# Optimization experiments

Hardware: AMD Instinct MI355X
Metric: run time of the kernel (lower is better)

Reference implementation:

```python
import jax, jax.numpy as jnp
import numpy as np

DIM = 256
WS = 7
NUM_HEADS = 8
NW = 4096


def _relative_position_index(ws: int) -> jnp.ndarray:
    coords = jnp.stack(jnp.meshgrid(jnp.arange(ws), jnp.arange(ws), indexing='ij'))  # [2, ws, ws]
    flat = coords.reshape(2, -1)                                # [2, N]
    rel = flat[:, :, None] - flat[:, None, :]                   # [2, N, N]
    rel = rel.transpose(1, 2, 0) + (ws - 1)                     # [N, N, 2]
    rel = rel.at[:, :, 0].multiply(2 * ws - 1)
    return rel.sum(-1).astype(jnp.int32)                        # [N, N]


def setup_inputs() -> dict:
    key = jax.random.key(0)
    ks = jax.random.split(key, 7)
    N = WS * WS
    x_win = jax.random.normal(ks[0], (NW, N, DIM), dtype=jnp.float32)
    attn_mask = jnp.zeros((NW, N, N), dtype=jnp.float32)
    w_qkv = jax.random.normal(ks[1], (3 * DIM, DIM), dtype=jnp.float32) * (1.0 / np.sqrt(DIM))
    b_qkv = jax.random.normal(ks[2], (3 * DIM,), dtype=jnp.float32) * 0.02
    w_proj = jax.random.normal(ks[3], (DIM, DIM), dtype=jnp.float32) * (1.0 / np.sqrt(DIM))
    b_proj = jax.random.normal(ks[4], (DIM,), dtype=jnp.float32) * 0.02
    bias_table = jax.random.normal(ks[5], ((2 * WS - 1) * (2 * WS - 1), NUM_HEADS), dtype=jnp.float32)
    rel_index = _relative_position_index(WS)
    return {
        'x_win': x_win, 'attn_mask': attn_mask,
        'w_qkv': w_qkv, 'b_qkv': b_qkv,
        'w_proj': w_proj, 'b_proj': b_proj,
        'bias_table': bias_table, 'rel_index': rel_index,
    }


def reference(x_win, attn_mask, w_qkv, b_qkv, w_proj, b_proj, bias_table, rel_index):
    nW, N, C = x_win.shape
    H = bias_table.shape[-1]
    head_dim = C // H
    scale = 1.0 / np.sqrt(head_dim).astype(np.float32)

    # QKV projection (eqx.nn.Linear: y = W x + b)
    qkv = jnp.einsum('wnc,oc->wno', x_win, w_qkv) + b_qkv      # [nW, N, 3C]
    q, k, v = jnp.split(qkv, 3, axis=-1)

    def to_heads(t):
        return t.reshape(nW, N, H, head_dim).transpose(0, 2, 1, 3)  # [nW, H, N, d]

    q, k, v = to_heads(q), to_heads(k), to_heads(v)

    attn = jnp.einsum('whnd,whmd->whnm', q * scale, k)          # [nW, H, N, N]

    # Gathered relative position bias -> [H, N, N]
    bias = bias_table[rel_index.reshape(-1)].reshape(N, N, H).transpose(2, 0, 1)
    attn = attn + bias[None, :, :, :] + attn_mask[:, None, :, :]
    attn = jax.nn.softmax(attn, axis=-1)

    out = jnp.einsum('whnm,whmd->whnd', attn, v)                # [nW, H, N, d]
    out = out.transpose(0, 2, 1, 3).reshape(nW, N, C)
    out = jnp.einsum('wnc,oc->wno', out, w_proj) + b_proj
    return out
```

## Files before the change

kernel.cpp:

```cpp
#include <hip/hip_runtime.h>
#include <hip/hip_bf16.h>

typedef __bf16 bf16;
typedef bf16 bf16x4 __attribute__((ext_vector_type(4)));
typedef bf16 bf16x8 __attribute__((ext_vector_type(8)));
typedef float f32x4 __attribute__((ext_vector_type(4)));

#define MFMA16(a, b, c) __builtin_amdgcn_mfma_f32_16x16x32_bf16((a), (b), (c), 0, 0, 0)

constexpr float kScale = 0.17677669529663687f;

constexpr int WQKV_OFF = 0;
constexpr int WPROJ_OFF = 393216;
constexpr int BIAS_OFF = 524288;
constexpr int BQKV_OFF = 601120;

constexpr int QK_OFF = 26240;
constexpr int QS = 410;
constexpr int LDS_BYTES = 78720;

__global__ void prep_kernel(const float* __restrict__ w_qkv, const float* __restrict__ b_qkv,
                            const float* __restrict__ w_proj, const float* __restrict__ bias_table,
                            const int* __restrict__ rel_index, char* __restrict__ ws) {
  int i = blockIdx.x * 256 + threadIdx.x;
  bf16* wqkvb = (bf16*)(ws + WQKV_OFF);
  bf16* wprojb = (bf16*)(ws + WPROJ_OFF);
  float* biasx = (float*)(ws + BIAS_OFF);
  float* bqs = (float*)(ws + BQKV_OFF);
  if (i < 196608) {
    float v = w_qkv[i];
    if (i < 65536) v *= kScale;
    wqkvb[i] = (bf16)v;
  } else if (i < 262144) {
    int j = i - 196608;
    wprojb[j] = (bf16)w_proj[j];
  } else if (i < 281352) {
    int j = i - 262144;
    int h = j / 2401, nm = j - h * 2401;
    int mm = nm / 49, nn = nm - mm * 49;
    biasx[j] = bias_table[rel_index[nn * 49 + mm] * 8 + h];
  } else if (i < 282120) {
    int j = i - 281352;
    bqs[j] = b_qkv[j] * (j < 256 ? kScale : 1.0f);
  }
}

__device__ __forceinline__ bf16x8 xpose8(f32x4 lo, f32x4 hi, int base, bool glow) {
  bf16x8 f;
#pragma unroll
  for (int i = 0; i < 4; ++i) {
    float a0 = __shfl(lo[i], base);
    float a1 = __shfl(lo[i], base + 16);
    float b0 = __shfl(hi[i], base);
    float b1 = __shfl(hi[i], base + 16);
    f[i] = (bf16)(glow ? a0 : b0);
    f[i + 4] = (bf16)(glow ? a1 : b1);
  }
  return f;
}

__global__ __launch_bounds__(256, 2) void attn_kernel(
    const float* __restrict__ x, const float* __restrict__ mask, const float* __restrict__ b_proj,
    const char* __restrict__ ws, float* __restrict__ out) {
  extern __shared__ char smem[];
  bf16* xb = (bf16*)(smem);
  bf16* qk = (bf16*)(smem + QK_OFF);
  float* outf = (float*)(smem + QK_OFF);

  const bf16* wqkvb = (const bf16*)(ws + WQKV_OFF);
  const bf16* wprojb = (const bf16*)(ws + WPROJ_OFF);
  const float* biasx = (const float*)(ws + BIAS_OFF);
  const float* bqs = (const float*)(ws + BQKV_OFF);

  const int tid = threadIdx.x;
  const int w = blockIdx.x;
  const int lane = tid & 63;
  const int wave = tid >> 6;
  const int g = lane >> 4;
  const int c = lane & 15;

  const float* xw = x + (size_t)w * 12544;

#pragma unroll
  for (int it = 0; it < 13; ++it) {
    int idx = it * 256 + tid;
    if (idx < 3136) {
      int n = idx >> 6, c4 = (idx & 63) << 2;
      float4 v = ((const float4*)xw)[idx];
      bf16x4 b4;
      b4[0] = (bf16)v.x; b4[1] = (bf16)v.y; b4[2] = (bf16)v.z; b4[3] = (bf16)v.w;
      *(bf16x4*)(xb + ((c4 >> 3) * QS + n * 8 + (c4 & 7))) = b4;
    }
  }
  __syncthreads();

  for (int qd = 0; qd < 2; ++qd) {
    const int ot0 = wave * 8 + qd * 4;
    f32x4 acc[4][4] = {};
#pragma unroll
    for (int ks = 0; ks < 8; ++ks) {
      bf16x8 b[4];
#pragma unroll
      for (int nt = 0; nt < 4; ++nt)
        b[nt] = *(const bf16x8*)(xb + (ks * 4 + g) * QS + c * 8 + nt * 128);
      bf16x8 a[4];
#pragma unroll
      for (int t = 0; t < 4; ++t)
        a[t] = *(const bf16x8*)(wqkvb + ((ot0 + t) * 16 + c) * 256 + ks * 32 + g * 8);
#pragma unroll
      for (int t = 0; t < 4; ++t)
#pragma unroll
        for (int nt = 0; nt < 4; ++nt) acc[t][nt] = MFMA16(a[t], b[nt], acc[t][nt]);
    }
#pragma unroll
    for (int t = 0; t < 4; ++t) {
      const int ot = ot0 + t;
      const int ob = ot * 16 + g * 4;
      const float bq0 = bqs[ob], bq1 = bqs[ob + 1], bq2 = bqs[ob + 2], bq3 = bqs[ob + 3];
      const int oc = ob >> 3, olow = ob & 7;
#pragma unroll
      for (int nt = 0; nt < 4; ++nt) {
        int n = nt * 16 + c;
        if (n < 50) {
          bool ok = (n < 49);
          bf16x4 pk;
          pk[0] = ok ? (bf16)(acc[t][nt][0] + bq0) : (bf16)0.f;
          pk[1] = ok ? (bf16)(acc[t][nt][1] + bq1) : (bf16)0.f;
          pk[2] = ok ? (bf16)(acc[t][nt][2] + bq2) : (bf16)0.f;
          pk[3] = ok ? (bf16)(acc[t][nt][3] + bq3) : (bf16)0.f;
          *(bf16x4*)(qk + (oc * QS + n * 8 + olow)) = pk;
        }
      }
    }
  }

  const int base = (g & 1) * 32 + c;
  const bool glow = (g < 2);

  bf16x8 va[2][2][2];
  {
    f32x4 acc[4][4] = {};
#pragma unroll
    for (int ks = 0; ks < 8; ++ks) {
      bf16x8 a[4];
#pragma unroll
      for (int mt = 0; mt < 4; ++mt)
        a[mt] = *(const bf16x8*)(xb + (ks * 4 + g) * QS + c * 8 + mt * 128);
      bf16x8 bw[4];
#pragma unroll
      for (int t = 0; t < 4; ++t)
        bw[t] = *(const bf16x8*)(wqkvb + (512 + (wave * 4 + t) * 16 + c) * 256 + ks * 32 + g * 8);
#pragma unroll
      for (int t = 0; t < 4; ++t)
#pragma unroll
        for (int mt = 0; mt < 4; ++mt) acc[t][mt] = MFMA16(a[mt], bw[t], acc[t][mt]);
    }
#pragma unroll
    for (int t = 0; t < 4; ++t) {
      const int o = 512 + (wave * 4 + t) * 16 + c;
      const float bv = bqs[o];
#pragma unroll
      for (int mt = 0; mt < 4; ++mt) {
        acc[t][mt][0] += bv; acc[t][mt][1] += bv; acc[t][mt][2] += bv; acc[t][mt][3] += bv;
      }
#pragma unroll
      for (int ks = 0; ks < 2; ++ks) {
        bf16x8 f = xpose8(acc[t][2 * ks], acc[t][2 * ks + 1], base, glow);
#pragma unroll
        for (int j = 0; j < 8; ++j) {
          int m = ks * 32 + g * 8 + j;
          if (m >= 49) f[j] = (bf16)0.f;
        }
        va[t >> 1][t & 1][ks] = f;
      }
    }
  }
  __syncthreads();

  const float* mk = mask + (size_t)w * 2401;

#pragma unroll
  for (int hh = 0; hh < 2; ++hh) {
    const int h = wave * 2 + hh;
    const float* bhT = biasx + h * 2401;

    bf16x8 qa[4], kb[4];
#pragma unroll
    for (int rt = 0; rt < 4; ++rt) {
      int n = rt * 16 + c; n = n > 49 ? 49 : n;
      qa[rt] = *(const bf16x8*)(qk + ((h * 4 + g) * QS + n * 8));
    }
#pragma unroll
    for (int mt = 0; mt < 4; ++mt) {
      int m = mt * 16 + c; m = m > 49 ? 49 : m;
      kb[mt] = *(const bf16x8*)(qk + ((32 + h * 4 + g) * QS + m * 8));
    }

    f32x4 s[4][4] = {};
#pragma unroll
    for (int mt = 0; mt < 4; ++mt)
#pragma unroll
      for (int nt = 0; nt < 4; ++nt) s[mt][nt] = MFMA16(kb[mt], qa[nt], s[mt][nt]);

    float bi[16], mi[16];
#define GATHER(NT)                                              \
    {                                                           \
      const int n_ = (NT) * 16 + c;                             \
      const int nc_ = n_ > 48 ? 48 : n_;                        \
      _Pragma("unroll") for (int mt = 0; mt < 4; ++mt)          \
        _Pragma("unroll") for (int i = 0; i < 4; ++i) {         \
          int m_ = mt * 16 + g * 4 + i;                         \
          int mc_ = m_ > 48 ? 48 : m_;                          \
          bi[mt * 4 + i] = bhT[mc_ * 49 + nc_];                 \
          mi[mt * 4 + i] = mk[nc_ * 49 + mc_];                  \
        }                                                       \
    }

    GATHER(0);
    f32x4 oacc[2][4] = {};
#pragma unroll
    for (int nt = 0; nt < 4; ++nt) {
      const int n = nt * 16 + c;
      const bool nok = (n < 49);
      float p[4][4];
      float sum = 0.f;
#pragma unroll
      for (int mt = 0; mt < 4; ++mt)
#pragma unroll
        for (int i = 0; i < 4; ++i) {
          int m = mt * 16 + g * 4 + i;
          float v = s[mt][nt][i] + bi[mt * 4 + i] + mi[mt * 4 + i];
          float pv = (nok && m < 49) ? __expf(v) : 0.f;
          p[mt][i] = pv;
          sum += pv;
        }
      sum += __shfl_xor(sum, 16);
      sum += __shfl_xor(sum, 32);
      float rinv = nok ? (1.0f / sum) : 0.0f;
#pragma unroll
      for (int mt = 0; mt < 4; ++mt)
#pragma unroll
        for (int i = 0; i < 4; ++i) p[mt][i] *= rinv;

      if (nt < 3) {
        if (nt == 0) GATHER(1);
        if (nt == 1) GATHER(2);
        if (nt == 2) GATHER(3);
      }

#pragma unroll
      for (int ks = 0; ks < 2; ++ks) {
        bf16x8 f;
#pragma unroll
        for (int j = 0; j < 8; ++j) {
          int src = ((g & 1) * 2 + (j >> 2)) * 16 + c;
          float vA = __shfl(p[2 * ks][j & 3], src);
          float vB = __shfl(p[2 * ks + 1][j & 3], src);
          f[j] = (bf16)(glow ? vA : vB);
        }
#pragma unroll
        for (int dt = 0; dt < 2; ++dt) oacc[dt][nt] = MFMA16(va[hh][dt][ks], f, oacc[dt][nt]);
      }
    }
#undef GATHER

#pragma unroll
    for (int dt = 0; dt < 2; ++dt) {
      int cb = h * 32 + dt * 16 + g * 4;
      int cc = cb >> 3, clow = cb & 7;
#pragma unroll
      for (int nt = 0; nt < 4; ++nt) {
        int n = nt * 16 + c;
        if (n < 49) {
          bf16x4 pk;
          pk[0] = (bf16)oacc[dt][nt][0]; pk[1] = (bf16)oacc[dt][nt][1];
          pk[2] = (bf16)oacc[dt][nt][2]; pk[3] = (bf16)oacc[dt][nt][3];
          *(bf16x4*)(xb + (cc * QS + n * 8 + clow)) = pk;
        }
      }
    }
  }
  __syncthreads();

  {
    f32x4 acc[4][4] = {};
#pragma unroll
    for (int ks = 0; ks < 8; ++ks) {
      bf16x8 a[4];
#pragma unroll
      for (int mt = 0; mt < 4; ++mt)
        a[mt] = *(const bf16x8*)(xb + (ks * 4 + g) * QS + c * 8 + mt * 128);
      bf16x8 bw[4];
#pragma unroll
      for (int t = 0; t < 4; ++t)
        bw[t] = *(const bf16x8*)(wprojb + ((wave * 4 + t) * 16 + c) * 256 + ks * 32 + g * 8);
#pragma unroll
      for (int t = 0; t < 4; ++t)
#pragma unroll
        for (int mt = 0; mt < 4; ++mt) acc[t][mt] = MFMA16(a[mt], bw[t], acc[t][mt]);
    }
#pragma unroll
    for (int t = 0; t < 4; ++t) {
      const int ct = wave * 4 + t;
      const float bp = b_proj[ct * 16 + c];
      const int co = ct * 16 + c, q = co >> 2, c3 = co & 3;
#pragma unroll
      for (int mt = 0; mt < 4; ++mt) {
#pragma unroll
        for (int i = 0; i < 4; ++i) {
          int n = mt * 16 + g * 4 + i;
          if (n < 49) outf[n * 256 + ((q ^ (n & 15)) << 2) + c3] = acc[t][mt][i] + bp;
        }
      }
    }
  }
  __syncthreads();

  float4* outw4 = (float4*)(out + (size_t)w * 12544);
  const float4* outf4 = (const float4*)outf;
#pragma unroll
  for (int it = 0; it < 13; ++it) {
    int f = it * 256 + tid;
    if (f < 3136) {
      int n = f >> 6, q = f & 63;
      outw4[f] = outf4[n * 64 + (q ^ (n & 15))];
    }
  }
}

extern "C" void kernel_launch(void* const* d_in, const int* in_sizes, int n_in,
                              void* d_out, int out_size, void* d_ws, size_t ws_size,
                              hipStream_t stream) {
  const float* x = (const float*)d_in[0];
  const float* mask = (const float*)d_in[1];
  const float* w_qkv = (const float*)d_in[2];
  const float* b_qkv = (const float*)d_in[3];
  const float* w_proj = (const float*)d_in[4];
  const float* b_proj = (const float*)d_in[5];
  const float* bias_table = (const float*)d_in[6];
  const int* rel_index = (const int*)d_in[7];
  float* out = (float*)d_out;
  char* ws = (char*)d_ws;

  (void)in_sizes; (void)n_in; (void)out_size; (void)ws_size;

  hipFuncSetAttribute((const void*)attn_kernel, hipFuncAttributeMaxDynamicSharedMemorySize,
                      LDS_BYTES);

  prep_kernel<<<1103, 256, 0, stream>>>(w_qkv, b_qkv, w_proj, bias_table, rel_index, ws);
  attn_kernel<<<4096, 256, LDS_BYTES, stream>>>(x, mask, b_proj, ws, out);
}
```

Measured before the change: 443.9 us.

## Compute Q/K per head in registers to shrink LDS and raise occupancy

Drops the LDS buffer that held the Q and K projections for all heads. Each wave now computes its head's Q and K tiles inside the head loop and transposes them in registers with shuffles. The output projection is split into two halves so its staging buffer fits in the x region. LDS drops from about 77KB to about 52KB and launch bounds go from 2 to 3 blocks per CU, aiming at higher occupancy and latency hiding. The trade-off is extra shuffle work, one more barrier per half, and tighter register limits that could cause spills.

```diff
diff --git a/kernel.cpp b/kernel.cpp
--- a/kernel.cpp
+++ b/kernel.cpp
@@ -15,9 +15,10 @@
 constexpr int BIAS_OFF = 524288;
 constexpr int BQKV_OFF = 601120;
 
-constexpr int QK_OFF = 26240;
+constexpr int A_OFF = 0;
+constexpr int B_OFF = 26240;
 constexpr int QS = 410;
-constexpr int LDS_BYTES = 78720;
+constexpr int LDS_BYTES = 52736;
 
 __global__ void prep_kernel(const float* __restrict__ w_qkv, const float* __restrict__ b_qkv,
                             const float* __restrict__ w_proj, const float* __restrict__ bias_table,
@@ -59,13 +60,13 @@
   return f;
 }
 
-__global__ __launch_bounds__(256, 2) void attn_kernel(
+__global__ __launch_bounds__(256, 3) void attn_kernel(
     const float* __restrict__ x, const float* __restrict__ mask, const float* __restrict__ b_proj,
     const char* __restrict__ ws, float* __restrict__ out) {
   extern __shared__ char smem[];
-  bf16* xb = (bf16*)(smem);
-  bf16* qk = (bf16*)(smem + QK_OFF);
-  float* outf = (float*)(smem + QK_OFF);
+  bf16* xb = (bf16*)(smem + A_OFF);
+  bf16* ao = (bf16*)(smem + B_OFF);
+  float* outf = (float*)(smem + A_OFF);
 
   const bf16* wqkvb = (const bf16*)(ws + WQKV_OFF);
   const bf16* wprojb = (const bf16*)(ws + WPROJ_OFF);
@@ -94,46 +95,6 @@
   }
   __syncthreads();
 
-  for (int qd = 0; qd < 2; ++qd) {
-    const int ot0 = wave * 8 + qd * 4;
-    f32x4 acc[4][4] = {};
-#pragma unroll
-    for (int ks = 0; ks < 8; ++ks) {
-      bf16x8 b[4];
-#pragma unroll
-      for (int nt = 0; nt < 4; ++nt)
-        b[nt] = *(const bf16x8*)(xb + (ks * 4 + g) * QS + c * 8 + nt * 128);
-      bf16x8 a[4];
-#pragma unroll
-      for (int t = 0; t < 4; ++t)
-        a[t] = *(const bf16x8*)(wqkvb + ((ot0 + t) * 16 + c) * 256 + ks * 32 + g * 8);
-#pragma unroll
-      for (int t = 0; t < 4; ++t)
-#pragma unroll
-        for (int nt = 0; nt < 4; ++nt) acc[t][nt] = MFMA16(a[t], b[nt], acc[t][nt]);
-    }
-#pragma unroll
-    for (int t = 0; t < 4; ++t) {
-      const int ot = ot0 + t;
-      const int ob = ot * 16 + g * 4;
-      const float bq0 = bqs[ob], bq1 = bqs[ob + 1], bq2 = bqs[ob + 2], bq3 = bqs[ob + 3];
-      const int oc = ob >> 3, olow = ob & 7;
-#pragma unroll
-      for (int nt = 0; nt < 4; ++nt) {
-        int n = nt * 16 + c;
-        if (n < 50) {
-          bool ok = (n < 49);
-          bf16x4 pk;
-          pk[0] = ok ? (bf16)(acc[t][nt][0] + bq0) : (bf16)0.f;
-          pk[1] = ok ? (bf16)(acc[t][nt][1] + bq1) : (bf16)0.f;
-          pk[2] = ok ? (bf16)(acc[t][nt][2] + bq2) : (bf16)0.f;
-          pk[3] = ok ? (bf16)(acc[t][nt][3] + bq3) : (bf16)0.f;
-          *(bf16x4*)(qk + (oc * QS + n * 8 + olow)) = pk;
-        }
-      }
-    }
-  }
-
   const int base = (g & 1) * 32 + c;
   const bool glow = (g < 2);
 
@@ -175,25 +136,49 @@
       }
     }
   }
-  __syncthreads();
 
   const float* mk = mask + (size_t)w * 2401;
 
-#pragma unroll
+#pragma unroll 1
   for (int hh = 0; hh < 2; ++hh) {
     const int h = wave * 2 + hh;
     const float* bhT = biasx + h * 2401;
 
     bf16x8 qa[4], kb[4];
-#pragma unroll
-    for (int rt = 0; rt < 4; ++rt) {
-      int n = rt * 16 + c; n = n > 49 ? 49 : n;
-      qa[rt] = *(const bf16x8*)(qk + ((h * 4 + g) * QS + n * 8));
-    }
-#pragma unroll
-    for (int mt = 0; mt < 4; ++mt) {
-      int m = mt * 16 + c; m = m > 49 ? 49 : m;
-      kb[mt] = *(const bf16x8*)(qk + ((32 + h * 4 + g) * QS + m * 8));
+    {
+      const int ob0 = 256 + h * 32;
+      const int ob2 = h * 32;
+      f32x4 acc[4][4] = {};
+#pragma unroll
+      for (int ks = 0; ks < 8; ++ks) {
+        bf16x8 b[4];
+#pragma unroll
+        for (int nt = 0; nt < 4; ++nt)
+          b[nt] = *(const bf16x8*)(xb + (ks * 4 + g) * QS + c * 8 + nt * 128);
+        bf16x8 a[4];
+        a[0] = *(const bf16x8*)(wqkvb + ((ob0 + c) * 256) + ks * 32 + g * 8);
+        a[1] = *(const bf16x8*)(wqkvb + ((ob0 + 16 + c) * 256) + ks * 32 + g * 8);
+        a[2] = *(const bf16x8*)(wqkvb + ((ob2 + c) * 256) + ks * 32 + g * 8);
+        a[3] = *(const bf16x8*)(wqkvb + ((ob2 + 16 + c) * 256) + ks * 32 + g * 8);
+#pragma unroll
+        for (int t = 0; t < 4; ++t)
+#pragma unroll
+          for (int nt = 0; nt < 4; ++nt) acc[t][nt] = MFMA16(a[t], b[nt], acc[t][nt]);
+      }
+#pragma unroll
+      for (int t = 0; t < 4; ++t) {
+        const int ob = (t < 2 ? ob0 + t * 16 : ob2 + (t - 2) * 16) + g * 4;
+#pragma unroll
+        for (int i = 0; i < 4; ++i) {
+          float bq = bqs[ob + i];
+#pragma unroll
+          for (int nt = 0; nt < 4; ++nt) acc[t][nt][i] += bq;
+        }
+      }
+#pragma unroll
+      for (int mt = 0; mt < 4; ++mt) kb[mt] = xpose8(acc[0][mt], acc[1][mt], base, glow);
+#pragma unroll
+      for (int rt = 0; rt < 4; ++rt) qa[rt] = xpose8(acc[2][rt], acc[3][rt], base, glow);
     }
 
     f32x4 s[4][4] = {};
@@ -275,56 +260,60 @@
           bf16x4 pk;
           pk[0] = (bf16)oacc[dt][nt][0]; pk[1] = (bf16)oacc[dt][nt][1];
           pk[2] = (bf16)oacc[dt][nt][2]; pk[3] = (bf16)oacc[dt][nt][3];
-          *(bf16x4*)(xb + (cc * QS + n * 8 + clow)) = pk;
+          *(bf16x4*)(ao + (cc * QS + n * 8 + clow)) = pk;
         }
       }
     }
   }
   __syncthreads();
 
-  {
-    f32x4 acc[4][4] = {};
+  float4* outw4 = (float4*)(out + (size_t)w * 12544);
+  const float4* outf4 = (const float4*)outf;
+#pragma unroll 1
+  for (int half = 0; half < 2; ++half) {
+    f32x4 acc[2][4] = {};
 #pragma unroll
     for (int ks = 0; ks < 8; ++ks) {
       bf16x8 a[4];
 #pragma unroll
       for (int mt = 0; mt < 4; ++mt)
-        a[mt] = *(const bf16x8*)(xb + (ks * 4 + g) * QS + c * 8 + mt * 128);
-      bf16x8 bw[4];
-#pragma unroll
-      for (int t = 0; t < 4; ++t)
-        bw[t] = *(const bf16x8*)(wprojb + ((wave * 4 + t) * 16 + c) * 256 + ks * 32 + g * 8);
-#pragma unroll
-      for (int t = 0; t < 4; ++t)
-#pragma unroll
-        for (int mt = 0; mt < 4; ++mt) acc[t][mt] = MFMA16(a[mt], bw[t], acc[t][mt]);
-    }
-#pragma unroll
-    for (int t = 0; t < 4; ++t) {
-      const int ct = wave * 4 + t;
+        a[mt] = *(const bf16x8*)(ao + (ks * 4 + g) * QS + c * 8 + mt * 128);
+      bf16x8 bw[2];
+#pragma unroll
+      for (int tt = 0; tt < 2; ++tt)
+        bw[tt] = *(const bf16x8*)(wprojb +
+                                  ((half * 8 + wave * 2 + tt) * 16 + c) * 256 + ks * 32 + g * 8);
+#pragma unroll
+      for (int tt = 0; tt < 2; ++tt)
+#pragma unroll
+        for (int mt = 0; mt < 4; ++mt) acc[tt][mt] = MFMA16(a[mt], bw[tt], acc[tt][mt]);
+    }
+#pragma unroll
+    for (int tt = 0; tt < 2; ++tt) {
+      const int ctl = wave * 2 + tt;
+      const int ct = half * 8 + ctl;
       const float bp = b_proj[ct * 16 + c];
-      const int co = ct * 16 + c, q = co >> 2, c3 = co & 3;
+      const int q = ctl * 4 + (c >> 2);
+      const int c3 = c & 3;
 #pragma unroll
       for (int mt = 0; mt < 4; ++mt) {
 #pragma unroll
         for (int i = 0; i < 4; ++i) {
           int n = mt * 16 + g * 4 + i;
-          if (n < 49) outf[n * 256 + ((q ^ (n & 15)) << 2) + c3] = acc[t][mt][i] + bp;
-        }
-      }
-    }
-  }
-  __syncthreads();
-
-  float4* outw4 = (float4*)(out + (size_t)w * 12544);
-  const float4* outf4 = (const float4*)outf;
-#pragma unroll
-  for (int it = 0; it < 13; ++it) {
-    int f = it * 256 + tid;
-    if (f < 3136) {
-      int n = f >> 6, q = f & 63;
-      outw4[f] = outf4[n * 64 + (q ^ (n & 15))];
-    }
+          if (n < 49) outf[n * 128 + ((q ^ (n & 7)) << 2) + c3] = acc[tt][mt][i] + bp;
+        }
+      }
+    }
+    __syncthreads();
+#pragma unroll
+    for (int it = 0; it < 7; ++it) {
+      int f = it * 256 + tid;
+      if (f < 1568) {
+        int n = f >> 5, q2 = f & 31;
+        outw4[n * 64 + half * 32 + q2] = outf4[n * 32 + (q2 ^ (n & 7))];
+      }
+    }
+    __syncthreads();
   }
 }
 
```

New measurement: 656.5 us. 47.9% more time.

## Split fused window attention into Q/K projection and attention kernels with global staging

Applied to the files above, without the earlier changes.

Q and K projections move to a separate kernel that writes bf16 Q/K tiles into workspace in chunks of windows. A second kernel recomputes V, then does attention and the output projection with a smaller LDS footprint, so it can run more blocks per CU. The aim is higher occupancy and less LDS pressure than the single fused kernel. The cost is extra global traffic for Q/K, a second read of x, and more launches. If the workspace is too small it falls back to the original fused kernel.

```diff
diff --git a/kernel.cpp b/kernel.cpp
--- a/kernel.cpp
+++ b/kernel.cpp
@@ -14,10 +14,10 @@
 constexpr int WPROJ_OFF = 393216;
 constexpr int BIAS_OFF = 524288;
 constexpr int BQKV_OFF = 601120;
-
-constexpr int QK_OFF = 26240;
+constexpr size_t QKG_OFF = 604672;
+
 constexpr int QS = 410;
-constexpr int LDS_BYTES = 78720;
+constexpr int GQS = 400;
 
 __global__ void prep_kernel(const float* __restrict__ w_qkv, const float* __restrict__ b_qkv,
                             const float* __restrict__ w_proj, const float* __restrict__ bias_table,
@@ -59,28 +59,7 @@
   return f;
 }
 
-__global__ __launch_bounds__(256, 2) void attn_kernel(
-    const float* __restrict__ x, const float* __restrict__ mask, const float* __restrict__ b_proj,
-    const char* __restrict__ ws, float* __restrict__ out) {
-  extern __shared__ char smem[];
-  bf16* xb = (bf16*)(smem);
-  bf16* qk = (bf16*)(smem + QK_OFF);
-  float* outf = (float*)(smem + QK_OFF);
-
-  const bf16* wqkvb = (const bf16*)(ws + WQKV_OFF);
-  const bf16* wprojb = (const bf16*)(ws + WPROJ_OFF);
-  const float* biasx = (const float*)(ws + BIAS_OFF);
-  const float* bqs = (const float*)(ws + BQKV_OFF);
-
-  const int tid = threadIdx.x;
-  const int w = blockIdx.x;
-  const int lane = tid & 63;
-  const int wave = tid >> 6;
-  const int g = lane >> 4;
-  const int c = lane & 15;
-
-  const float* xw = x + (size_t)w * 12544;
-
+__device__ __forceinline__ void stage_x(const float* __restrict__ xw, bf16* xb, int tid) {
 #pragma unroll
   for (int it = 0; it < 13; ++it) {
     int idx = it * 256 + tid;
@@ -92,6 +71,309 @@
       *(bf16x4*)(xb + ((c4 >> 3) * QS + n * 8 + (c4 & 7))) = b4;
     }
   }
+}
+
+__global__ __launch_bounds__(256, 4) void qk_kernel(
+    const float* __restrict__ x, const char* __restrict__ ws, bf16* __restrict__ qkg, int w0) {
+  __shared__ bf16 xb[32 * QS + 128];
+  const bf16* wqkvb = (const bf16*)(ws + WQKV_OFF);
+  const float* bqs = (const float*)(ws + BQKV_OFF);
+
+  const int tid = threadIdx.x;
+  const int lane = tid & 63;
+  const int wave = tid >> 6;
+  const int g = lane >> 4;
+  const int c = lane & 15;
+
+  stage_x(x + (size_t)(w0 + blockIdx.x) * 12544, xb, tid);
+  __syncthreads();
+
+  bf16* qw = qkg + (size_t)blockIdx.x * 25600;
+
+  for (int qd = 0; qd < 2; ++qd) {
+    const int ot0 = wave * 8 + qd * 4;
+    f32x4 acc[4][4] = {};
+#pragma unroll
+    for (int ks = 0; ks < 8; ++ks) {
+      bf16x8 b[4];
+#pragma unroll
+      for (int nt = 0; nt < 4; ++nt)
+        b[nt] = *(const bf16x8*)(xb + (ks * 4 + g) * QS + c * 8 + nt * 128);
+      bf16x8 a[4];
+#pragma unroll
+      for (int t = 0; t < 4; ++t)
+        a[t] = *(const bf16x8*)(wqkvb + ((ot0 + t) * 16 + c) * 256 + ks * 32 + g * 8);
+#pragma unroll
+      for (int t = 0; t < 4; ++t)
+#pragma unroll
+        for (int nt = 0; nt < 4; ++nt) acc[t][nt] = MFMA16(a[t], b[nt], acc[t][nt]);
+    }
+#pragma unroll
+    for (int t = 0; t < 4; ++t) {
+      const int ot = ot0 + t;
+      const int ob = ot * 16 + g * 4;
+      const float bq0 = bqs[ob], bq1 = bqs[ob + 1], bq2 = bqs[ob + 2], bq3 = bqs[ob + 3];
+      const int oc = ob >> 3, olow = ob & 7;
+#pragma unroll
+      for (int nt = 0; nt < 4; ++nt) {
+        int n = nt * 16 + c;
+        if (n < 50) {
+          bool ok = (n < 49);
+          bf16x4 pk;
+          pk[0] = ok ? (bf16)(acc[t][nt][0] + bq0) : (bf16)0.f;
+          pk[1] = ok ? (bf16)(acc[t][nt][1] + bq1) : (bf16)0.f;
+          pk[2] = ok ? (bf16)(acc[t][nt][2] + bq2) : (bf16)0.f;
+          pk[3] = ok ? (bf16)(acc[t][nt][3] + bq3) : (bf16)0.f;
+          *(bf16x4*)(qw + (oc * GQS + n * 8 + olow)) = pk;
+        }
+      }
+    }
+  }
+}
+
+__global__ __launch_bounds__(256, 3) void attn2_kernel(
+    const float* __restrict__ x, const float* __restrict__ mask, const float* __restrict__ b_proj,
+    const char* __restrict__ ws, const bf16* __restrict__ qkg, float* __restrict__ out, int w0) {
+  __shared__ char smem[26240 + 25088 + 128];
+  bf16* xb = (bf16*)smem;
+  float* outf = (float*)(smem + 26240);
+
+  const bf16* wqkvb = (const bf16*)(ws + WQKV_OFF);
+  const bf16* wprojb = (const bf16*)(ws + WPROJ_OFF);
+  const float* biasx = (const float*)(ws + BIAS_OFF);
+  const float* bqs = (const float*)(ws + BQKV_OFF);
+
+  const int tid = threadIdx.x;
+  const int w = w0 + blockIdx.x;
+  const int lane = tid & 63;
+  const int wave = tid >> 6;
+  const int g = lane >> 4;
+  const int c = lane & 15;
+
+  stage_x(x + (size_t)w * 12544, xb, tid);
+  __syncthreads();
+
+  const int base = (g & 1) * 32 + c;
+  const bool glow = (g < 2);
+
+  bf16x8 va[2][2][2];
+  {
+    f32x4 acc[4][4] = {};
+#pragma unroll
+    for (int ks = 0; ks < 8; ++ks) {
+      bf16x8 a[4];
+#pragma unroll
+      for (int mt = 0; mt < 4; ++mt)
+        a[mt] = *(const bf16x8*)(xb + (ks * 4 + g) * QS + c * 8 + mt * 128);
+      bf16x8 bw[4];
+#pragma unroll
+      for (int t = 0; t < 4; ++t)
+        bw[t] = *(const bf16x8*)(wqkvb + (512 + (wave * 4 + t) * 16 + c) * 256 + ks * 32 + g * 8);
+#pragma unroll
+      for (int t = 0; t < 4; ++t)
+#pragma unroll
+        for (int mt = 0; mt < 4; ++mt) acc[t][mt] = MFMA16(a[mt], bw[t], acc[t][mt]);
+    }
+#pragma unroll
+    for (int t = 0; t < 4; ++t) {
+      const int o = 512 + (wave * 4 + t) * 16 + c;
+      const float bv = bqs[o];
+#pragma unroll
+      for (int mt = 0; mt < 4; ++mt) {
+        acc[t][mt][0] += bv; acc[t][mt][1] += bv; acc[t][mt][2] += bv; acc[t][mt][3] += bv;
+      }
+#pragma unroll
+      for (int ks = 0; ks < 2; ++ks) {
+        bf16x8 f = xpose8(acc[t][2 * ks], acc[t][2 * ks + 1], base, glow);
+#pragma unroll
+        for (int j = 0; j < 8; ++j) {
+          int m = ks * 32 + g * 8 + j;
+          if (m >= 49) f[j] = (bf16)0.f;
+        }
+        va[t >> 1][t & 1][ks] = f;
+      }
+    }
+  }
+  __syncthreads();
+  bf16* ao = xb;
+
+  const float* mk = mask + (size_t)w * 2401;
+  const bf16* qw = qkg + (size_t)blockIdx.x * 25600;
+
+#pragma unroll
+  for (int hh = 0; hh < 2; ++hh) {
+    const int h = wave * 2 + hh;
+    const float* bhT = biasx + h * 2401;
+
+    bf16x8 qa[4], kb[4];
+#pragma unroll
+    for (int rt = 0; rt < 4; ++rt) {
+      int n = rt * 16 + c; n = n > 49 ? 49 : n;
+      qa[rt] = *(const bf16x8*)(qw + (h * 4 + g) * GQS + n * 8);
+    }
+#pragma unroll
+    for (int mt = 0; mt < 4; ++mt) {
+      int m = mt * 16 + c; m = m > 49 ? 49 : m;
+      kb[mt] = *(const bf16x8*)(qw + ((32 + h * 4 + g) * GQS + m * 8));
+    }
+
+    f32x4 s[4][4] = {};
+#pragma unroll
+    for (int mt = 0; mt < 4; ++mt)
+#pragma unroll
+      for (int nt = 0; nt < 4; ++nt) s[mt][nt] = MFMA16(kb[mt], qa[nt], s[mt][nt]);
+
+    float bi[16], mi[16];
+#define GATHER(NT)                                              \
+    {                                                           \
+      const int n_ = (NT) * 16 + c;                             \
+      const int nc_ = n_ > 48 ? 48 : n_;                        \
+      _Pragma("unroll") for (int mt = 0; mt < 4; ++mt)          \
+        _Pragma("unroll") for (int i = 0; i < 4; ++i) {         \
+          int m_ = mt * 16 + g * 4 + i;                         \
+          int mc_ = m_ > 48 ? 48 : m_;                          \
+          bi[mt * 4 + i] = bhT[mc_ * 49 + nc_];                 \
+          mi[mt * 4 + i] = mk[nc_ * 49 + mc_];                  \
+        }                                                       \
+    }
+
+    GATHER(0);
+    f32x4 oacc[2][4] = {};
+#pragma unroll
+    for (int nt = 0; nt < 4; ++nt) {
+      const int n = nt * 16 + c;
+      const bool nok = (n < 49);
+      float p[4][4];
+      float sum = 0.f;
+#pragma unroll
+      for (int mt = 0; mt < 4; ++mt)
+#pragma unroll
+        for (int i = 0; i < 4; ++i) {
+          int m = mt * 16 + g * 4 + i;
+          float v = s[mt][nt][i] + bi[mt * 4 + i] + mi[mt * 4 + i];
+          float pv = (nok && m < 49) ? __expf(v) : 0.f;
+          p[mt][i] = pv;
+          sum += pv;
+        }
+      sum += __shfl_xor(sum, 16);
+      sum += __shfl_xor(sum, 32);
+      float rinv = nok ? (1.0f / sum) : 0.0f;
+#pragma unroll
+      for (int mt = 0; mt < 4; ++mt)
+#pragma unroll
+        for (int i = 0; i < 4; ++i) p[mt][i] *= rinv;
+
+      if (nt < 3) {
+        if (nt == 0) GATHER(1);
+        if (nt == 1) GATHER(2);
+        if (nt == 2) GATHER(3);
+      }
+
+#pragma unroll
+      for (int ks = 0; ks < 2; ++ks) {
+        bf16x8 f;
+#pragma unroll
+        for (int j = 0; j < 8; ++j) {
+          int src = ((g & 1) * 2 + (j >> 2)) * 16 + c;
+          float vA = __shfl(p[2 * ks][j & 3], src);
+          float vB = __shfl(p[2 * ks + 1][j & 3], src);
+          f[j] = (bf16)(glow ? vA : vB);
+        }
+#pragma unroll
+        for (int dt = 0; dt < 2; ++dt) oacc[dt][nt] = MFMA16(va[hh][dt][ks], f, oacc[dt][nt]);
+      }
+    }
+#undef GATHER
+
+#pragma unroll
+    for (int dt = 0; dt < 2; ++dt) {
+      int cb = h * 32 + dt * 16 + g * 4;
+      int cc = cb >> 3, clow = cb & 7;
+#pragma unroll
+      for (int nt = 0; nt < 4; ++nt) {
+        int n = nt * 16 + c;
+        if (n < 49) {
+          bf16x4 pk;
+          pk[0] = (bf16)oacc[dt][nt][0]; pk[1] = (bf16)oacc[dt][nt][1];
+          pk[2] = (bf16)oacc[dt][nt][2]; pk[3] = (bf16)oacc[dt][nt][3];
+          *(bf16x4*)(ao + (cc * QS + n * 8 + clow)) = pk;
+        }
+      }
+    }
+  }
+  __syncthreads();
+
+  float4* outw4 = (float4*)(out + (size_t)w * 12544);
+  const float4* outf4 = (const float4*)outf;
+#pragma unroll 1
+  for (int half = 0; half < 2; ++half) {
+    f32x4 acc[2][4] = {};
+#pragma unroll
+    for (int ks = 0; ks < 8; ++ks) {
+      bf16x8 a[4];
+#pragma unroll
+      for (int mt = 0; mt < 4; ++mt)
+        a[mt] = *(const bf16x8*)(ao + (ks * 4 + g) * QS + c * 8 + mt * 128);
+      bf16x8 bw[2];
+#pragma unroll
+      for (int tt = 0; tt < 2; ++tt)
+        bw[tt] = *(const bf16x8*)(wprojb +
+                                  ((half * 8 + wave * 2 + tt) * 16 + c) * 256 + ks * 32 + g * 8);
+#pragma unroll
+      for (int tt = 0; tt < 2; ++tt)
+#pragma unroll
+        for (int mt = 0; mt < 4; ++mt) acc[tt][mt] = MFMA16(a[mt], bw[tt], acc[tt][mt]);
+    }
+#pragma unroll
+    for (int tt = 0; tt < 2; ++tt) {
+      const int ctl = wave * 2 + tt;
+      const int ct = half * 8 + ctl;
+      const float bp = b_proj[ct * 16 + c];
+      const int q = ctl * 4 + (c >> 2);
+      const int c3 = c & 3;
+#pragma unroll
+      for (int mt = 0; mt < 4; ++mt) {
+#pragma unroll
+        for (int i = 0; i < 4; ++i) {
+          int n = mt * 16 + g * 4 + i;
+          if (n < 49) outf[n * 128 + ((q ^ (n & 7)) << 2) + c3] = acc[tt][mt][i] + bp;
+        }
+      }
+    }
+    __syncthreads();
+#pragma unroll
+    for (int it = 0; it < 7; ++it) {
+      int f = it * 256 + tid;
+      if (f < 1568) {
+        int n = f >> 5, q2 = f & 31;
+        outw4[n * 64 + half * 32 + q2] = outf4[n * 32 + (q2 ^ (n & 7))];
+      }
+    }
+    __syncthreads();
+  }
+}
+
+__global__ __launch_bounds__(256, 2) void fused_kernel(
+    const float* __restrict__ x, const float* __restrict__ mask, const float* __restrict__ b_proj,
+    const char* __restrict__ ws, float* __restrict__ out) {
+  extern __shared__ char dsm[];
+  bf16* xb = (bf16*)(dsm);
+  bf16* qk = (bf16*)(dsm + 26240);
+  float* outf = (float*)(dsm + 26240);
+
+  const bf16* wqkvb = (const bf16*)(ws + WQKV_OFF);
+  const bf16* wprojb = (const bf16*)(ws + WPROJ_OFF);
+  const float* biasx = (const float*)(ws + BIAS_OFF);
+  const float* bqs = (const float*)(ws + BQKV_OFF);
+
+  const int tid = threadIdx.x;
+  const int w = blockIdx.x;
+  const int lane = tid & 63;
+  const int wave = tid >> 6;
+  const int g = lane >> 4;
+  const int c = lane & 15;
+
+  stage_x(x + (size_t)w * 12544, xb, tid);
   __syncthreads();
 
   for (int qd = 0; qd < 2; ++qd) {
@@ -342,11 +624,24 @@
   float* out = (float*)d_out;
   char* ws = (char*)d_ws;
 
-  (void)in_sizes; (void)n_in; (void)out_size; (void)ws_size;
-
-  hipFuncSetAttribute((const void*)attn_kernel, hipFuncAttributeMaxDynamicSharedMemorySize,
-                      LDS_BYTES);
+  (void)in_sizes; (void)n_in; (void)out_size;
 
   prep_kernel<<<1103, 256, 0, stream>>>(w_qkv, b_qkv, w_proj, bias_table, rel_index, ws);
-  attn_kernel<<<4096, 256, LDS_BYTES, stream>>>(x, mask, b_proj, ws, out);
+
+  size_t avail = ws_size > QKG_OFF ? ws_size - QKG_OFF : 0;
+  long cwl = (long)(avail / 51200);
+  int cw = cwl > 1024 ? 1024 : (int)cwl;
+
+  if (cw >= 512) {
+    bf16* qkg = (bf16*)(ws + QKG_OFF);
+    for (int s = 0; s < 4096; s += cw) {
+      int nb = (4096 - s) < cw ? (4096 - s) : cw;
+      qk_kernel<<<nb, 256, 0, stream>>>(x, ws, qkg, s);
+      attn2_kernel<<<nb, 256, 0, stream>>>(x, mask, b_proj, ws, qkg, out, s);
+    }
+  } else {
+    hipFuncSetAttribute((const void*)fused_kernel, hipFuncAttributeMaxDynamicSharedMemorySize,
+                        78720);
+    fused_kernel<<<4096, 256, 78720, stream>>>(x, mask, b_proj, ws, out);
+  }
 }
```

New measurement: 685.8 us. 54.5% more time.

## Pre-permute bias and mask into MFMA fragment order for coalesced loads

Applied to the files above, without the earlier changes.

The relative-position bias table is now expanded in the prep kernel into a per-head, per-lane layout that matches the MFMA accumulator fragments. A new kernel converts each window's mask to bf16 in the same fragment order. The attention kernel can then read bias and mask with contiguous lane-indexed loads instead of transposed, strided gathers. The cost is an extra full pass over the mask, with a read and a bf16 write to the workspace, plus reduced mask precision.

```diff
diff --git a/kernel.cpp b/kernel.cpp
--- a/kernel.cpp
+++ b/kernel.cpp
@@ -12,10 +12,10 @@
 
 constexpr int WQKV_OFF = 0;
 constexpr int WPROJ_OFF = 393216;
-constexpr int BIAS_OFF = 524288;
-constexpr int BQKV_OFF = 601120;
-
-constexpr int QK_OFF = 26240;
+constexpr int BIASR_OFF = 524288;
+constexpr int BQKV_OFF = 655360;
+constexpr size_t MASKR_OFF = 658432;
+
 constexpr int QS = 410;
 constexpr int LDS_BYTES = 78720;
 
@@ -25,7 +25,7 @@
   int i = blockIdx.x * 256 + threadIdx.x;
   bf16* wqkvb = (bf16*)(ws + WQKV_OFF);
   bf16* wprojb = (bf16*)(ws + WPROJ_OFF);
-  float* biasx = (float*)(ws + BIAS_OFF);
+  float* biasr = (float*)(ws + BIASR_OFF);
   float* bqs = (float*)(ws + BQKV_OFF);
   if (i < 196608) {
     float v = w_qkv[i];
@@ -34,14 +34,38 @@
   } else if (i < 262144) {
     int j = i - 196608;
     wprojb[j] = (bf16)w_proj[j];
-  } else if (i < 281352) {
+  } else if (i < 294912) {
     int j = i - 262144;
-    int h = j / 2401, nm = j - h * 2401;
-    int mm = nm / 49, nn = nm - mm * 49;
-    biasx[j] = bias_table[rel_index[nn * 49 + mm] * 8 + h];
-  } else if (i < 282120) {
-    int j = i - 281352;
+    int h = j >> 12, r = j & 4095;
+    int lane = r & 63, q = r >> 6;
+    int i2 = q & 3, p = q >> 2, mt = p & 3, nt = p >> 2;
+    int nn = nt * 16 + (lane & 15); nn = nn > 48 ? 48 : nn;
+    int mm = mt * 16 + (lane >> 4) * 4 + i2; mm = mm > 48 ? 48 : mm;
+    biasr[j] = bias_table[rel_index[nn * 49 + mm] * 8 + h];
+  } else if (i < 295680) {
+    int j = i - 294912;
     bqs[j] = b_qkv[j] * (j < 256 ? kScale : 1.0f);
+  }
+}
+
+__global__ void maskr_kernel(const float* __restrict__ mask, char* __restrict__ ws) {
+  const int w = blockIdx.x;
+  const float* mk = mask + (size_t)w * 2401;
+  bf16* mr = (bf16*)(ws + MASKR_OFF) + (size_t)w * 4096;
+#pragma unroll
+  for (int rep = 0; rep < 4; ++rep) {
+    int o = (rep * 256 + threadIdx.x) * 4;
+    int q = o >> 6;
+    int i2 = q & 3, p = q >> 2, mt = p & 3, nt = p >> 2;
+    bf16x4 v;
+#pragma unroll
+    for (int j = 0; j < 4; ++j) {
+      int L = (o & 63) + j;
+      int nn = nt * 16 + (L & 15); nn = nn > 48 ? 48 : nn;
+      int mm = mt * 16 + (L >> 4) * 4 + i2; mm = mm > 48 ? 48 : mm;
+      v[j] = (bf16)mk[nn * 49 + mm];
+    }
+    *(bf16x4*)(mr + o) = v;
   }
 }
 
@@ -60,16 +84,16 @@
 }
 
 __global__ __launch_bounds__(256, 2) void attn_kernel(
-    const float* __restrict__ x, const float* __restrict__ mask, const float* __restrict__ b_proj,
+    const float* __restrict__ x, const float* __restrict__ b_proj,
     const char* __restrict__ ws, float* __restrict__ out) {
   extern __shared__ char smem[];
   bf16* xb = (bf16*)(smem);
-  bf16* qk = (bf16*)(smem + QK_OFF);
-  float* outf = (float*)(smem + QK_OFF);
+  bf16* qk = (bf16*)(smem + 26240);
+  float* outf = (float*)(smem + 26240);
 
   const bf16* wqkvb = (const bf16*)(ws + WQKV_OFF);
   const bf16* wprojb = (const bf16*)(ws + WPROJ_OFF);
-  const float* biasx = (const float*)(ws + BIAS_OFF);
+  const float* biasr = (const float*)(ws + BIASR_OFF);
   const float* bqs = (const float*)(ws + BQKV_OFF);
 
   const int tid = threadIdx.x;
@@ -177,12 +201,12 @@
   }
   __syncthreads();
 
-  const float* mk = mask + (size_t)w * 2401;
+  const bf16* mkR = (const bf16*)(ws + MASKR_OFF) + (size_t)w * 4096;
 
 #pragma unroll
   for (int hh = 0; hh < 2; ++hh) {
     const int h = wave * 2 + hh;
-    const float* bhT = biasx + h * 2401;
+    const float* bhR = biasr + h * 4096;
 
     bf16x8 qa[4], kb[4];
 #pragma unroll
@@ -203,17 +227,14 @@
       for (int nt = 0; nt < 4; ++nt) s[mt][nt] = MFMA16(kb[mt], qa[nt], s[mt][nt]);
 
     float bi[16], mi[16];
-#define GATHER(NT)                                              \
-    {                                                           \
-      const int n_ = (NT) * 16 + c;                             \
-      const int nc_ = n_ > 48 ? 48 : n_;                        \
-      _Pragma("unroll") for (int mt = 0; mt < 4; ++mt)          \
-        _Pragma("unroll") for (int i = 0; i < 4; ++i) {         \
-          int m_ = mt * 16 + g * 4 + i;                         \
-          int mc_ = m_ > 48 ? 48 : m_;                          \
-          bi[mt * 4 + i] = bhT[mc_ * 49 + nc_];                 \
-          mi[mt * 4 + i] = mk[nc_ * 49 + mc_];                  \
-        }                                                       \
+#define GATHER(NT)                                                        \
+    {                                                                     \
+      _Pragma("unroll") for (int mt = 0; mt < 4; ++mt)                    \
+        _Pragma("unroll") for (int i = 0; i < 4; ++i) {                   \
+          int off = (((NT) * 4 + mt) * 4 + i) * 64 + lane;                \
+          bi[mt * 4 + i] = bhR[off];                                      \
+          mi[mt * 4 + i] = (float)mkR[off];                               \
+        }                                                                 \
     }
 
     GATHER(0);
@@ -347,6 +368,7 @@
   hipFuncSetAttribute((const void*)attn_kernel, hipFuncAttributeMaxDynamicSharedMemorySize,
                       LDS_BYTES);
 
-  prep_kernel<<<1103, 256, 0, stream>>>(w_qkv, b_qkv, w_proj, bias_table, rel_index, ws);
-  attn_kernel<<<4096, 256, LDS_BYTES, stream>>>(x, mask, b_proj, ws, out);
-}
+  prep_kernel<<<1155, 256, 0, stream>>>(w_qkv, b_qkv, w_proj, bias_table, rel_index, ws);
+  maskr_kernel<<<4096, 256, 0, stream>>>(mask, ws);
+  attn_kernel<<<4096, 256, LDS_BYTES, stream>>>(x, b_proj, ws, out);
+}
```

Result: slower. 482.4 us (+8.7%).
